# Performance work log

Measured on AMD Instinct MI355X. Metric: run time of the kernel, lower is better.

Reference implementation:

```python
import jax, jax.numpy as jnp
import numpy as np

B, N, IN_DIM = 16, 2048, 64
DIM, HEADS, DEPTH, K, NCLS = 512, 8, 4, 256, 2
DH = DIM // HEADS
EPS = 1e-5


def layernorm(h, s, b):
    mu = jnp.mean(h, axis=-1, keepdims=True)
    var = jnp.mean(jnp.square(h - mu), axis=-1, keepdims=True)
    return (h - mu) * jax.lax.rsqrt(var + EPS) * s + b


def setup_inputs() -> dict:
    key = jax.random.key(0)
    ks = jax.random.split(key, 20)
    w = 0.02
    L = DEPTH
    return {
        "x": jax.random.normal(ks[0], (B, N, IN_DIM), jnp.float32),
        "emb_w": jax.random.normal(ks[1], (IN_DIM, DIM), jnp.float32) * w,
        "emb_b": jnp.zeros((DIM,), jnp.float32),
        "pos": jax.random.normal(ks[2], (1, N, DIM), jnp.float32) * w,
        "ln1_s": jnp.ones((L, DIM), jnp.float32),
        "ln1_b": jnp.zeros((L, DIM), jnp.float32),
        "wq": jax.random.normal(ks[3], (L, DIM, DIM), jnp.float32) * w,
        "wk": jax.random.normal(ks[4], (L, DIM, DIM), jnp.float32) * w,
        "wv": jax.random.normal(ks[5], (L, DIM, DIM), jnp.float32) * w,
        "pk": jax.random.normal(ks[6], (L, N, K), jnp.float32) * (1.0 / np.sqrt(N)),
        "pv": jax.random.normal(ks[7], (L, N, K), jnp.float32) * (1.0 / np.sqrt(N)),
        "wo": jax.random.normal(ks[8], (L, DIM, DIM), jnp.float32) * w,
        "wo_b": jnp.zeros((L, DIM), jnp.float32),
        "ln2_s": jnp.ones((L, DIM), jnp.float32),
        "ln2_b": jnp.zeros((L, DIM), jnp.float32),
        "w1": jax.random.normal(ks[9], (L, DIM, 4 * DIM), jnp.float32) * w,
        "b1": jnp.zeros((L, 4 * DIM), jnp.float32),
        "w2": jax.random.normal(ks[10], (L, 4 * DIM, DIM), jnp.float32) * w,
        "b2": jnp.zeros((L, DIM), jnp.float32),
        "fc_w": jax.random.normal(ks[11], (DIM, NCLS), jnp.float32) * w,
        "fc_b": jnp.zeros((NCLS,), jnp.float32),
    }


def reference(x, emb_w, emb_b, pos, ln1_s, ln1_b, wq, wk, wv, pk, pv, wo, wo_b,
              ln2_s, ln2_b, w1, b1, w2, b2, fc_w, fc_b):
    scale = DH ** -0.5
    h = x @ emb_w + emb_b + pos  # [B,N,DIM]
    for i in range(DEPTH):
        # Linformer self-attention (PreNorm + residual)
        z = layernorm(h, ln1_s[i], ln1_b[i])
        q = (z @ wq[i]).reshape(B, N, HEADS, DH)
        k = z @ wk[i]  # [B,N,DIM]
        v = z @ wv[i]
        # low-rank projection along sequence: [B,N,DIM] x [N,K] -> [B,K,DIM]
        kp = jnp.einsum('bnd,nk->bkd', k, pk[i]).reshape(B, K, HEADS, DH)
        vp = jnp.einsum('bnd,nk->bkd', v, pv[i]).reshape(B, K, HEADS, DH)
        dots = jnp.einsum('bnhd,bkhd->bhnk', q, kp) * scale
        attn = jax.nn.softmax(dots, axis=-1)
        out = jnp.einsum('bhnk,bkhd->bnhd', attn, vp).reshape(B, N, DIM)
        h = h + out @ wo[i] + wo_b[i]
        # FeedForward (PreNorm + residual)
        z = layernorm(h, ln2_s[i], ln2_b[i])
        h = h + jax.nn.gelu(z @ w1[i] + b1[i]) @ w2[i] + b2[i]
    pooled = jnp.mean(h, axis=1)  # [B,DIM]
    return pooled @ fc_w + fc_b  # [B,NCLS]
```

## Files before the change

### kernel.cpp

```cpp
#include <hip/hip_runtime.h>
#include <math.h>

#define B_    16
#define N_    2048
#define INDIM 64
#define DIM_  512
#define HEADS 8
#define DEPTH 4
#define KLIN  256
#define NCLS  2
#define DH    64
#define EPSF  1e-5f

typedef __attribute__((ext_vector_type(8))) short short8v;
typedef __attribute__((ext_vector_type(4))) short short4v;
typedef __attribute__((ext_vector_type(4))) float f32x4;

#define SBAR() __builtin_amdgcn_sched_barrier(0)

__device__ __forceinline__ short f2bf(float f) {
  unsigned u = __float_as_uint(f);
  u += 0x7FFFu + ((u >> 16) & 1u);
  return (short)(u >> 16);
}

__device__ __forceinline__ float wave_sum(float v) {
  #pragma unroll
  for (int o = 32; o > 0; o >>= 1) v += __shfl_xor(v, o);
  return v;
}

__device__ __forceinline__ float gelu_tanh(float x) {
  float u = x * (1.5957691216057308f + 0.07135481627f * x * x);
  return x / (1.f + __expf(-u));
}

__device__ __forceinline__ void gl_lds16(const short* g, short* l) {
  __builtin_amdgcn_global_load_lds(
      (const __attribute__((address_space(1))) unsigned int*)g,
      (__attribute__((address_space(3))) unsigned int*)l, 16, 0, 0);
}

__global__ __launch_bounds__(256) void tconv_k(const float* __restrict__ src,
                                               short* __restrict__ dst, int R,
                                               int C, long long sSrc,
                                               long long sDst) {
  __shared__ float tile[32][33];
  int c0 = blockIdx.x * 32, r0 = blockIdx.y * 32;
  src += (long long)blockIdx.z * sSrc;
  dst += (long long)blockIdx.z * sDst;
  int tx = threadIdx.x & 31, ty = threadIdx.x >> 5;
  #pragma unroll
  for (int rr = 0; rr < 4; ++rr)
    tile[ty + rr * 8][tx] = src[(long long)(r0 + ty + rr * 8) * C + c0 + tx];
  __syncthreads();
  #pragma unroll
  for (int rr = 0; rr < 4; ++rr) {
    int c = ty + rr * 8;
    dst[(long long)(c0 + c) * R + r0 + tx] = f2bf(tile[tx][c]);
  }
}

__global__ __launch_bounds__(256) void cconv_k(const float* __restrict__ src,
                                               short* __restrict__ dst,
                                               int n8) {
  int i = blockIdx.x * 256 + threadIdx.x;
  if (i < n8) {
    const float* s = src + (long long)i * 8;
    float4 a = *(const float4*)s, c = *(const float4*)(s + 4);
    short8v o = {f2bf(a.x), f2bf(a.y), f2bf(a.z), f2bf(a.w),
                 f2bf(c.x), f2bf(c.y), f2bf(c.z), f2bf(c.w)};
    *(short8v*)(dst + (long long)i * 8) = o;
  }
}

__global__ __launch_bounds__(256) void tpose_k(const short* __restrict__ src,
                                               short* __restrict__ dst, int R,
                                               int C, long long sSrc,
                                               long long sDst) {
  __shared__ __align__(16) short tile[64][72];
  int c0 = blockIdx.x * 64, r0 = blockIdx.y * 64;
  src += (long long)blockIdx.z * sSrc;
  dst += (long long)blockIdx.z * sDst;
  int t = threadIdx.x;
  #pragma unroll
  for (int rep = 0; rep < 2; ++rep) {
    int row = rep * 32 + (t >> 3), c8 = (t & 7) * 8;
    *(short8v*)&tile[row][c8] =
        *(const short8v*)(src + (long long)(r0 + row) * C + c0 + c8);
  }
  __syncthreads();
  #pragma unroll
  for (int rep = 0; rep < 2; ++rep) {
    int c = rep * 32 + (t >> 3), r8 = (t & 7) * 8;
    short8v o;
    #pragma unroll
    for (int j = 0; j < 8; ++j) o[j] = tile[r8 + j][c];
    *(short8v*)(dst + (long long)(c0 + c) * R + r0 + r8) = o;
  }
}

__global__ __launch_bounds__(256) void ln_k(const float* __restrict__ h,
                                            const float* __restrict__ s,
                                            const float* __restrict__ b,
                                            short* __restrict__ z) {
  int lane = threadIdx.x & 63;
  long long row = ((long long)blockIdx.x << 2) + (threadIdx.x >> 6);
  const float* hr = h + row * DIM_ + lane * 8;
  float4 a = *(const float4*)hr;
  float4 c = *(const float4*)(hr + 4);
  float sum = a.x + a.y + a.z + a.w + c.x + c.y + c.z + c.w;
  sum = wave_sum(sum);
  float mu = sum * (1.f / DIM_);
  float d[8] = {a.x - mu, a.y - mu, a.z - mu, a.w - mu,
                c.x - mu, c.y - mu, c.z - mu, c.w - mu};
  float vs = 0.f;
  #pragma unroll
  for (int i = 0; i < 8; ++i) vs += d[i] * d[i];
  vs = wave_sum(vs);
  float rstd = rsqrtf(vs * (1.f / DIM_) + EPSF);
  const float* sp = s + lane * 8;
  const float* bp = b + lane * 8;
  float4 s0 = *(const float4*)sp, s1 = *(const float4*)(sp + 4);
  float4 b0 = *(const float4*)bp, b1 = *(const float4*)(bp + 4);
  float o[8];
  o[0] = d[0] * rstd * s0.x + b0.x; o[1] = d[1] * rstd * s0.y + b0.y;
  o[2] = d[2] * rstd * s0.z + b0.z; o[3] = d[3] * rstd * s0.w + b0.w;
  o[4] = d[4] * rstd * s1.x + b1.x; o[5] = d[5] * rstd * s1.y + b1.y;
  o[6] = d[6] * rstd * s1.z + b1.z; o[7] = d[7] * rstd * s1.w + b1.w;
  short8v ov = {f2bf(o[0]), f2bf(o[1]), f2bf(o[2]), f2bf(o[3]),
                f2bf(o[4]), f2bf(o[5]), f2bf(o[6]), f2bf(o[7])};
  *(short8v*)(z + row * DIM_ + lane * 8) = ov;
}

template <int OUTBF, int BM, int BN>
__global__ __launch_bounds__(256) void gemm_bf(
    const short* __restrict__ A, const short* __restrict__ Bsrc,
    const float* __restrict__ bias, const float* __restrict__ resid,
    void* __restrict__ Cv, int M, int N, int K, int lda, int ldb, int ldc,
    long long sAb, long long sBb, long long sCb, int dualThresh,
    long long dualOff, int epi, int resMod) {
  constexpr int MT = BM / 32;
  constexpr int NT = BN / 32;
  constexpr int NLD = BM / 32 + BN / 32;
  int zz = blockIdx.z;
  A += (long long)zz * sAb;
  Bsrc += (long long)zz * sBb;
  int bm = blockIdx.y * BM, bn = blockIdx.x * BN;
  if (dualThresh && bm >= dualThresh) Bsrc += dualOff;
  int t = threadIdx.x;
  __shared__ __align__(16) short Alds[2][BM * 64];
  __shared__ __align__(16) short Blds[2][BN * 64];
  int lane = t & 63, wid = t >> 6;
  int lr = lane & 15, q = lane >> 4;
  int wm = (wid >> 1) * (BM / 2), wn = (wid & 1) * (BN / 2);
  int rl = lane >> 3;
  int cs = (lane & 7) ^ rl;
  f32x4 acc[MT][NT] = {};

  auto stage = [&](int buf, int k0) {
    #pragma unroll
    for (int i = 0; i < BM / 32; ++i) {
      int rb = i * 32 + wid * 8;
      gl_lds16(A + (long long)(bm + rb + rl) * lda + k0 + cs * 8,
               &Alds[buf][rb * 64]);
    }
    #pragma unroll
    for (int i = 0; i < BN / 32; ++i) {
      int rb = i * 32 + wid * 8;
      gl_lds16(Bsrc + (long long)(bn + rb + rl) * ldb + k0 + cs * 8,
               &Blds[buf][rb * 64]);
    }
  };

  stage(0, 0);
  int cur = 0;
  for (int k0 = 0; k0 < K; k0 += 64, cur ^= 1) {
    if (k0 + 64 < K) {
      stage(cur ^ 1, k0 + 64);
      SBAR();
      asm volatile("s_waitcnt vmcnt(%0)" ::"n"(NLD) : "memory");
    } else {
      SBAR();
      asm volatile("s_waitcnt vmcnt(0)" ::: "memory");
    }
    __builtin_amdgcn_s_barrier();
    SBAR();
    #pragma unroll
    for (int kk2 = 0; kk2 < 2; ++kk2) {
      short8v af[MT], bfr[NT];
      #pragma unroll
      for (int mi = 0; mi < MT; ++mi)
        af[mi] = *(const short8v*)&Alds[cur][(wm + mi * 16 + lr) * 64 +
                                             (((kk2 << 2) | q) ^ (lr & 7)) * 8];
      #pragma unroll
      for (int ni = 0; ni < NT; ++ni)
        bfr[ni] = *(const short8v*)&Blds[cur][(wn + ni * 16 + lr) * 64 +
                                              (((kk2 << 2) | q) ^ (lr & 7)) * 8];
      #pragma unroll
      for (int mi = 0; mi < MT; ++mi)
        #pragma unroll
        for (int ni = 0; ni < NT; ++ni)
          acc[mi][ni] = __builtin_amdgcn_mfma_f32_16x16x32_bf16(
              bfr[ni], af[mi], acc[mi][ni], 0, 0, 0);
    }
    SBAR();
    __builtin_amdgcn_s_barrier();
  }

  #pragma unroll
  for (int mi = 0; mi < MT; ++mi) {
    int m = bm + wm + mi * 16 + lr;
    int rm = (epi == 2 && resMod) ? (m % resMod) : m;
    #pragma unroll
    for (int ni = 0; ni < NT; ++ni) {
      int nb = bn + wn + ni * 16 + q * 4;
      f32x4 v = acc[mi][ni];
      if (epi >= 1) {
        float4 bb = *(const float4*)(bias + nb);
        v[0] += bb.x; v[1] += bb.y; v[2] += bb.z; v[3] += bb.w;
      }
      if (epi == 2) {
        float4 rr = *(const float4*)(resid + (long long)rm * ldc + nb);
        v[0] += rr.x; v[1] += rr.y; v[2] += rr.z; v[3] += rr.w;
      } else if (epi == 3) {
        v[0] = gelu_tanh(v[0]); v[1] = gelu_tanh(v[1]);
        v[2] = gelu_tanh(v[2]); v[3] = gelu_tanh(v[3]);
      }
      long long base = (long long)zz * sCb + (long long)m * ldc + nb;
      if (OUTBF) {
        short4v o = {f2bf(v[0]), f2bf(v[1]), f2bf(v[2]), f2bf(v[3])};
        *(short4v*)((short*)Cv + base) = o;
      } else {
        *(float4*)((float*)Cv + base) = make_float4(v[0], v[1], v[2], v[3]);
      }
    }
  }
}

template <int OUTBF, int BN, int EPI>
__global__ __launch_bounds__(512, 2) void gemm8(
    const short* __restrict__ A, const short* __restrict__ Bt,
    const float* __restrict__ bias, const float* __restrict__ resid,
    void* __restrict__ Cv, int M, int N, int K) {
  constexpr int BM = 256;
  constexpr int WCOL = BN / 4;
  constexpr int NT = WCOL / 16;
  constexpr int NTH = NT / 2;
  constexpr int LB = BN / 128;
  __shared__ __align__(16) short Alds[2][BM * 64];
  __shared__ __align__(16) short Blds[2][BN * 64];
  const int tid = threadIdx.x;
  const int lane = tid & 63, wid = tid >> 6;
  const int lr = lane & 15, q = lane >> 4;
  const int wm = (wid >> 2) * 128, wn = (wid & 3) * WCOL;
  const int rl = lane >> 3, cs = (lane & 7) ^ rl;
  const int bm = blockIdx.y * BM, bn = blockIdx.x * BN;
  const short* Ag = A + (long long)bm * K + cs * 8;
  const short* Bg = Bt + (long long)bn * K + cs * 8;
  f32x4 acc[8][NT] = {};

  auto stageA = [&](int slot, int h, int k0) {
    #pragma unroll
    for (int j = 0; j < 2; ++j) {
      int rb = h * 128 + j * 64 + wid * 8;
      gl_lds16(Ag + (long long)(rb + rl) * K + k0, &Alds[slot][rb * 64]);
    }
  };
  auto stageB = [&](int slot, int h, int k0) {
    #pragma unroll
    for (int j = 0; j < LB; ++j) {
      int rb = h * (BN / 2) + j * 64 + wid * 8;
      gl_lds16(Bg + (long long)(rb + rl) * K + k0, &Blds[slot][rb * 64]);
    }
  };
  auto rd = [&](const short* Ls, int row, int kk) -> short8v {
    return *(const short8v*)&Ls[row * 64 + ((((kk << 2) | q) ^ (lr & 7)) << 3)];
  };
  auto mfma4 = [&](short8v (&af)[4][2], short8v (&bf)[NTH][2], int mo, int no) {
    #pragma unroll
    for (int mi = 0; mi < 4; ++mi)
      #pragma unroll
      for (int ni = 0; ni < NTH; ++ni)
        #pragma unroll
        for (int kk = 0; kk < 2; ++kk)
          acc[mo + mi][no + ni] = __builtin_amdgcn_mfma_f32_16x16x32_bf16(
              bf[ni][kk], af[mi][kk], acc[mo + mi][no + ni], 0, 0, 0);
  };

  const int T = K >> 6;
  stageA(0, 0, 0); stageA(0, 1, 0); stageB(0, 0, 0); stageB(0, 1, 0);
  if (T > 1) {
    stageA(1, 0, 64);
    SBAR();
    asm volatile("s_waitcnt vmcnt(2)" ::: "memory");
  } else {
    SBAR();
    asm volatile("s_waitcnt vmcnt(0)" ::: "memory");
  }
  __builtin_amdgcn_s_barrier();

  for (int tt = 0; tt < T; ++tt) {
    const int s = tt & 1, ns = s ^ 1;
    const int kn = (tt + 1) << 6, kn2 = (tt + 2) << 6;
    const short* Als = Alds[s];
    const short* Bls = Blds[s];
    short8v af0[4][2], af1[4][2], bf0[NTH][2], bf1[NTH][2];
    SBAR();
    #pragma unroll
    for (int mi = 0; mi < 4; ++mi)
      #pragma unroll
      for (int kk = 0; kk < 2; ++kk)
        af0[mi][kk] = rd(Als, wm + mi * 16 + lr, kk);
    #pragma unroll
    for (int ni = 0; ni < NTH; ++ni)
      #pragma unroll
      for (int kk = 0; kk < 2; ++kk)
        bf0[ni][kk] = rd(Bls, wn + ni * 16 + lr, kk);
    if (tt + 1 < T) stageA(ns, 1, kn);
    if (BN == 256) asm volatile("s_waitcnt lgkmcnt(8)" ::: "memory");
    SBAR();
    __builtin_amdgcn_s_barrier();
    asm volatile("s_waitcnt lgkmcnt(0)" ::: "memory");
    SBAR();
    __builtin_amdgcn_s_setprio(1);
    mfma4(af0, bf0, 0, 0);
    __builtin_amdgcn_s_setprio(0);
    SBAR();
    __builtin_amdgcn_s_barrier();
    SBAR();
    #pragma unroll
    for (int ni = 0; ni < NTH; ++ni)
      #pragma unroll
      for (int kk = 0; kk < 2; ++kk)
        bf1[ni][kk] = rd(Bls, wn + (NTH + ni) * 16 + lr, kk);
    SBAR();
    __builtin_amdgcn_s_barrier();
    asm volatile("s_waitcnt lgkmcnt(0)" ::: "memory");
    SBAR();
    __builtin_amdgcn_s_setprio(1);
    mfma4(af0, bf1, 0, NTH);
    __builtin_amdgcn_s_setprio(0);
    SBAR();
    __builtin_amdgcn_s_barrier();
    SBAR();
    #pragma unroll
    for (int mi = 0; mi < 4; ++mi)
      #pragma unroll
      for (int kk = 0; kk < 2; ++kk)
        af1[mi][kk] = rd(Als, wm + 64 + mi * 16 + lr, kk);
    if (tt + 1 < T) stageB(ns, 0, kn);
    SBAR();
    __builtin_amdgcn_s_barrier();
    asm volatile("s_waitcnt lgkmcnt(0)" ::: "memory");
    SBAR();
    __builtin_amdgcn_s_setprio(1);
    mfma4(af1, bf0, 4, 0);
    __builtin_amdgcn_s_setprio(0);
    SBAR();
    __builtin_amdgcn_s_barrier();
    SBAR();
    if (tt + 1 < T) stageB(ns, 1, kn);
    if (tt + 2 < T) stageA(s, 0, kn2);
    SBAR();
    __builtin_amdgcn_s_barrier();
    __builtin_amdgcn_s_setprio(1);
    mfma4(af1, bf1, 4, NTH);
    __builtin_amdgcn_s_setprio(0);
    if (tt + 2 < T) {
      SBAR();
      asm volatile("s_waitcnt vmcnt(2)" ::: "memory");
    } else if (tt + 1 < T) {
      SBAR();
      asm volatile("s_waitcnt vmcnt(0)" ::: "memory");
    }
    SBAR();
    __builtin_amdgcn_s_barrier();
  }

  #pragma unroll
  for (int mi = 0; mi < 8; ++mi) {
    int m = bm + wm + mi * 16 + lr;
    #pragma unroll
    for (int nj = 0; nj < NT; ++nj) {
      int nb = bn + wn + nj * 16 + q * 4;
      f32x4 v = acc[mi][nj];
      if (EPI >= 1) {
        float4 bb = *(const float4*)(bias + nb);
        v[0] += bb.x; v[1] += bb.y; v[2] += bb.z; v[3] += bb.w;
      }
      if (EPI == 2) {
        float4 rr = *(const float4*)(resid + (long long)m * N + nb);
        v[0] += rr.x; v[1] += rr.y; v[2] += rr.z; v[3] += rr.w;
      } else if (EPI == 3) {
        v[0] = gelu_tanh(v[0]); v[1] = gelu_tanh(v[1]);
        v[2] = gelu_tanh(v[2]); v[3] = gelu_tanh(v[3]);
      }
      long long base = (long long)m * N + nb;
      if (OUTBF) {
        short4v o = {f2bf(v[0]), f2bf(v[1]), f2bf(v[2]), f2bf(v[3])};
        *(short4v*)((short*)Cv + base) = o;
      } else {
        *(float4*)((float*)Cv + base) = make_float4(v[0], v[1], v[2], v[3]);
      }
    }
  }
}

__global__ __launch_bounds__(256) void attn_k(short* __restrict__ qc,
                                              const short* __restrict__ kvp,
                                              float scale) {
  int n0 = blockIdx.x * 64, hh = blockIdx.y, b = blockIdx.z;
  int t = threadIdx.x;
  int lane = t & 63, w = t >> 6;
  int lr = lane & 15, qd = lane >> 4;

  __shared__ __align__(16) short Qlds[64][72];
  __shared__ __align__(16) short Kbuf[256 * 72];
  __shared__ __align__(16) short Vt[64][264];
  auto Klds = (short(*)[72])Kbuf;
  auto Plds = (short(*)[264])Kbuf;

  short* qptr = qc + (long long)b * N_ * DIM_ + hh * DH;
  const short* kptr = kvp + (long long)b * 2 * KLIN * DIM_ + hh * DH;
  const short* vptr = kptr + (long long)KLIN * DIM_;

  #pragma unroll
  for (int rep = 0; rep < 2; ++rep) {
    int L = rep * 256 + t, row = L >> 3, c8 = (L & 7) << 3;
    *(short8v*)&Qlds[row][c8] =
        *(const short8v*)(qptr + (long long)(n0 + row) * DIM_ + c8);
  }
  #pragma unroll
  for (int rep = 0; rep < 8; ++rep) {
    int L = rep * 256 + t, row = L >> 3, c8 = (L & 7) << 3;
    *(short8v*)&Klds[row][c8] =
        *(const short8v*)(kptr + (long long)row * DIM_ + c8);
  }
  #pragma unroll
  for (int rep = 0; rep < 4; ++rep) {
    int key0 = rep * 64 + (t >> 4) * 4, dh0 = (t & 15) * 4;
    short4v a0 = *(const short4v*)(vptr + (long long)(key0 + 0) * DIM_ + dh0);
    short4v a1 = *(const short4v*)(vptr + (long long)(key0 + 1) * DIM_ + dh0);
    short4v a2 = *(const short4v*)(vptr + (long long)(key0 + 2) * DIM_ + dh0);
    short4v a3 = *(const short4v*)(vptr + (long long)(key0 + 3) * DIM_ + dh0);
    short4v w0 = {a0[0], a1[0], a2[0], a3[0]};
    short4v w1 = {a0[1], a1[1], a2[1], a3[1]};
    short4v w2 = {a0[2], a1[2], a2[2], a3[2]};
    short4v w3 = {a0[3], a1[3], a2[3], a3[3]};
    *(short4v*)&Vt[dh0 + 0][key0] = w0;
    *(short4v*)&Vt[dh0 + 1][key0] = w1;
    *(short4v*)&Vt[dh0 + 2][key0] = w2;
    *(short4v*)&Vt[dh0 + 3][key0] = w3;
  }
  __syncthreads();

  short8v qa0 = *(const short8v*)&Qlds[16 * w + lr][qd * 8];
  short8v qa1 = *(const short8v*)&Qlds[16 * w + lr][32 + qd * 8];
  f32x4 sacc[16];
  #pragma unroll
  for (int nt = 0; nt < 16; ++nt) {
    short8v b0 = *(const short8v*)&Klds[nt * 16 + lr][qd * 8];
    short8v b1 = *(const short8v*)&Klds[nt * 16 + lr][32 + qd * 8];
    f32x4 acc = {};
    acc = __builtin_amdgcn_mfma_f32_16x16x32_bf16(qa0, b0, acc, 0, 0, 0);
    acc = __builtin_amdgcn_mfma_f32_16x16x32_bf16(qa1, b1, acc, 0, 0, 0);
    sacc[nt] = acc;
  }

  #pragma unroll
  for (int r = 0; r < 4; ++r) {
    float m = -1e30f;
    #pragma unroll
    for (int nt = 0; nt < 16; ++nt) {
      sacc[nt][r] *= scale;
      m = fmaxf(m, sacc[nt][r]);
    }
    #pragma unroll
    for (int o = 1; o < 16; o <<= 1) m = fmaxf(m, __shfl_xor(m, o));
    float rs = 0.f;
    #pragma unroll
    for (int nt = 0; nt < 16; ++nt) {
      float e = __expf(sacc[nt][r] - m);
      sacc[nt][r] = e;
      rs += e;
    }
    #pragma unroll
    for (int o = 1; o < 16; o <<= 1) rs += __shfl_xor(rs, o);
    float inv = 1.f / rs;
    #pragma unroll
    for (int nt = 0; nt < 16; ++nt) sacc[nt][r] *= inv;
  }

  __syncthreads();
  #pragma unroll
  for (int nt = 0; nt < 16; ++nt)
    #pragma unroll
    for (int r = 0; r < 4; ++r)
      Plds[16 * w + qd * 4 + r][nt * 16 + lr] = f2bf(sacc[nt][r]);
  __syncthreads();

  f32x4 out[4] = {};
  #pragma unroll
  for (int k0 = 0; k0 < 8; ++k0) {
    short8v ap = *(const short8v*)&Plds[16 * w + lr][k0 * 32 + qd * 8];
    #pragma unroll
    for (int n2 = 0; n2 < 4; ++n2) {
      short8v bv = *(const short8v*)&Vt[n2 * 16 + lr][k0 * 32 + qd * 8];
      out[n2] =
          __builtin_amdgcn_mfma_f32_16x16x32_bf16(bv, ap, out[n2], 0, 0, 0);
    }
  }

  long long rowoff = (long long)(n0 + 16 * w + lr) * DIM_;
  #pragma unroll
  for (int n2 = 0; n2 < 4; ++n2) {
    short4v o = {f2bf(out[n2][0]), f2bf(out[n2][1]), f2bf(out[n2][2]),
                 f2bf(out[n2][3])};
    *(short4v*)(qptr + rowoff + n2 * 16 + qd * 4) = o;
  }
}

__global__ __launch_bounds__(256) void pool1_k(const float* __restrict__ h,
                                               float* __restrict__ partial) {
  int stripe = blockIdx.x, b = blockIdx.y;
  int c4 = (threadIdx.x & 127) * 4, half = threadIdx.x >> 7;
  const float* base =
      h + ((long long)b * N_ + stripe * 128 + half * 64) * DIM_ + c4;
  float4 acc = {0.f, 0.f, 0.f, 0.f};
  for (int r = 0; r < 64; ++r) {
    float4 v = *(const float4*)(base + (long long)r * DIM_);
    acc.x += v.x; acc.y += v.y; acc.z += v.z; acc.w += v.w;
  }
  __shared__ float red[512];
  if (half == 1) *(float4*)&red[c4] = acc;
  __syncthreads();
  if (half == 0) {
    float4 o = *(const float4*)&red[c4];
    o.x += acc.x; o.y += acc.y; o.z += acc.z; o.w += acc.w;
    *(float4*)&partial[((long long)b * 16 + stripe) * DIM_ + c4] = o;
  }
}
__global__ __launch_bounds__(256) void pool2_k(const float* __restrict__ partial,
                                               float* __restrict__ pooled) {
  int b = blockIdx.x;
  for (int c = threadIdx.x; c < DIM_; c += 256) {
    float s = 0.f;
    for (int k = 0; k < 16; ++k) s += partial[((long long)b * 16 + k) * DIM_ + c];
    pooled[b * DIM_ + c] = s * (1.f / N_);
  }
}

__global__ __launch_bounds__(64) void fc_k(const float* __restrict__ pooled,
                                           const float* __restrict__ fc_w,
                                           const float* __restrict__ fc_b,
                                           float* __restrict__ out) {
  int t = threadIdx.x;
  if (t < B_ * NCLS) {
    int b = t >> 1, c = t & 1;
    float s = fc_b[c];
    for (int d = 0; d < DIM_; ++d)
      s += pooled[b * DIM_ + d] * fc_w[d * NCLS + c];
    out[t] = s;
  }
}

extern "C" void kernel_launch(void* const* d_in, const int* in_sizes, int n_in,
                              void* d_out, int out_size, void* d_ws,
                              size_t ws_size, hipStream_t stream) {
  const float* x     = (const float*)d_in[0];
  const float* emb_w = (const float*)d_in[1];
  const float* emb_b = (const float*)d_in[2];
  const float* pos   = (const float*)d_in[3];
  const float* ln1_s = (const float*)d_in[4];
  const float* ln1_b = (const float*)d_in[5];
  const float* wq    = (const float*)d_in[6];
  const float* wk    = (const float*)d_in[7];
  const float* wv    = (const float*)d_in[8];
  const float* pk    = (const float*)d_in[9];
  const float* pv    = (const float*)d_in[10];
  const float* wo    = (const float*)d_in[11];
  const float* wo_b  = (const float*)d_in[12];
  const float* ln2_s = (const float*)d_in[13];
  const float* ln2_b = (const float*)d_in[14];
  const float* w1    = (const float*)d_in[15];
  const float* b1    = (const float*)d_in[16];
  const float* w2    = (const float*)d_in[17];
  const float* b2    = (const float*)d_in[18];
  const float* fc_w  = (const float*)d_in[19];
  const float* fc_b  = (const float*)d_in[20];
  float* out = (float*)d_out;

  const bool big = ws_size >= (size_t)230 * 1024 * 1024;
  const int acb = big ? 16 : 8;
  const long long acrows = (long long)acb * N_;
  const int frows = big ? 16384 : 8192;

  char* P = (char*)d_ws;
  float* h = (float*)P;            P += (long long)B_ * N_ * DIM_ * 4;
  short* zc = (short*)P;           P += acrows * DIM_ * 2;
  short* qc = (short*)P;           P += acrows * DIM_ * 2;
  short* ffnmid = zc;
  short* zcT = (short*)P;          P += acrows * DIM_ * 2;
  short* zln = zcT;
  short* zp = (short*)P;           P += (long long)acb * 2 * KLIN * DIM_ * 2;
  short* kvp = (short*)P;          P += (long long)acb * 2 * KLIN * DIM_ * 2;
  short* wq_t  = (short*)P;  P += (long long)DEPTH * DIM_ * DIM_ * 2;
  short* wkv_t = (short*)P;  P += (long long)DEPTH * 2 * DIM_ * DIM_ * 2;
  short* wo_t  = (short*)P;  P += (long long)DEPTH * DIM_ * DIM_ * 2;
  short* w1_t  = (short*)P;  P += (long long)DEPTH * 4 * DIM_ * DIM_ * 2;
  short* w2_t  = (short*)P;  P += (long long)DEPTH * 4 * DIM_ * DIM_ * 2;
  short* pkv_t = (short*)P;  P += (long long)DEPTH * 2 * KLIN * N_ * 2;
  short* emb_wt = (short*)P; P += (long long)DIM_ * INDIM * 2;
  short* x_bf  = (short*)P;  P += (long long)B_ * N_ * INDIM * 2;
  float* partial = (float*)P; P += (long long)B_ * 16 * DIM_ * 4;
  float* pooled  = (float*)P;

  const float scale = 0.125f;
  const long long WQS = (long long)DIM_ * DIM_;
  const long long KVS = (long long)2 * KLIN * DIM_;

  auto tconv = [&](const float* s, short* d, int R, int C, long long ss,
                   long long sd, int b) {
    hipLaunchKernelGGL(tconv_k, dim3(C / 32, R / 32, b), dim3(256), 0, stream,
                       s, d, R, C, ss, sd);
  };
  tconv(wq, wq_t, DIM_, DIM_, WQS, WQS, DEPTH);
  tconv(wk, wkv_t, DIM_, DIM_, WQS, 2 * WQS, DEPTH);
  tconv(wv, wkv_t + WQS, DIM_, DIM_, WQS, 2 * WQS, DEPTH);
  tconv(wo, wo_t, DIM_, DIM_, WQS, WQS, DEPTH);
  tconv(w1, w1_t, DIM_, 4 * DIM_, 4 * WQS, 4 * WQS, DEPTH);
  tconv(w2, w2_t, 4 * DIM_, DIM_, 4 * WQS, 4 * WQS, DEPTH);
  tconv(pk, pkv_t, N_, KLIN, (long long)N_ * KLIN, (long long)2 * KLIN * N_, DEPTH);
  tconv(pv, pkv_t + (long long)KLIN * N_, N_, KLIN, (long long)N_ * KLIN,
        (long long)2 * KLIN * N_, DEPTH);
  tconv(emb_w, emb_wt, INDIM, DIM_, 0, 0, 1);
  hipLaunchKernelGGL(cconv_k, dim3((B_ * N_ * INDIM / 8 + 255) / 256),
                     dim3(256), 0, stream, x, x_bf, B_ * N_ * INDIM / 8);

  hipLaunchKernelGGL((gemm_bf<0, 128, 128>), dim3(DIM_ / 128, B_ * N_ / 128, 1),
                     dim3(256), 0, stream, x_bf, emb_wt, emb_b, pos, (void*)h,
                     B_ * N_, DIM_, INDIM, INDIM, INDIM, DIM_, 0LL, 0LL, 0LL,
                     0, 0LL, 2, N_);

  for (int i = 0; i < DEPTH; ++i) {
    const short* wq_i  = wq_t + i * WQS;
    const short* wkv_i = wkv_t + i * 2 * WQS;
    const short* wo_i  = wo_t + i * WQS;
    const short* w1_i  = w1_t + (long long)i * 4 * WQS;
    const short* w2_i  = w2_t + (long long)i * 4 * WQS;
    const short* pkv_i = pkv_t + (long long)i * 2 * KLIN * N_;

    for (int c = 0; c < B_ / acb; ++c) {
      float* hc = h + (long long)c * acrows * DIM_;
      hipLaunchKernelGGL(ln_k, dim3(acrows / 4), dim3(256), 0, stream, hc,
                         ln1_s + i * DIM_, ln1_b + i * DIM_, zc);
      hipLaunchKernelGGL(tpose_k, dim3(DIM_ / 64, N_ / 64, acb), dim3(256), 0,
                         stream, zc, zcT, N_, DIM_, (long long)N_ * DIM_,
                         (long long)DIM_ * N_);
      hipLaunchKernelGGL((gemm8<1, 256, 0>),
                         dim3(DIM_ / 256, (int)(acrows / 256), 1), dim3(512), 0,
                         stream, zc, wq_i, nullptr, nullptr, (void*)qc,
                         (int)acrows, DIM_, DIM_);
      hipLaunchKernelGGL((gemm_bf<1, 64, 128>), dim3(DIM_ / 128, 512 / 64, acb),
                         dim3(256), 0, stream, pkv_i, zcT, nullptr, nullptr,
                         (void*)zp, 512, DIM_, N_, N_, N_, DIM_, 0LL,
                         (long long)DIM_ * N_, KVS, 0, 0LL, 0, 0);
      hipLaunchKernelGGL((gemm_bf<1, 64, 128>), dim3(DIM_ / 128, 512 / 64, acb),
                         dim3(256), 0, stream, zp, wkv_i, nullptr, nullptr,
                         (void*)kvp, 512, DIM_, DIM_, DIM_, DIM_, DIM_, KVS,
                         0LL, KVS, KLIN, (long long)WQS, 0, 0);
      hipLaunchKernelGGL(attn_k, dim3(N_ / 64, HEADS, acb), dim3(256), 0,
                         stream, qc, kvp, scale);
      hipLaunchKernelGGL((gemm8<0, 256, 2>),
                         dim3(DIM_ / 256, (int)(acrows / 256), 1), dim3(512), 0,
                         stream, qc, wo_i, wo_b + i * DIM_, hc, (void*)hc,
                         (int)acrows, DIM_, DIM_);
    }

    for (int r0 = 0; r0 < B_ * N_; r0 += frows) {
      float* hr = h + (long long)r0 * DIM_;
      hipLaunchKernelGGL(ln_k, dim3(frows / 4), dim3(256), 0, stream, hr,
                         ln2_s + i * DIM_, ln2_b + i * DIM_, zln);
      hipLaunchKernelGGL((gemm8<1, 256, 3>),
                         dim3(4 * DIM_ / 256, frows / 256, 1), dim3(512), 0,
                         stream, zln, w1_i, b1 + (long long)i * 4 * DIM_,
                         nullptr, (void*)ffnmid, frows, 4 * DIM_, DIM_);
      hipLaunchKernelGGL((gemm8<0, 128, 2>),
                         dim3(DIM_ / 128, frows / 256, 1), dim3(512), 0,
                         stream, ffnmid, w2_i, b2 + (long long)i * DIM_, hr,
                         (void*)hr, frows, DIM_, 4 * DIM_);
    }
  }

  hipLaunchKernelGGL(pool1_k, dim3(16, B_), dim3(256), 0, stream, h, partial);
  hipLaunchKernelGGL(pool2_k, dim3(B_), dim3(256), 0, stream, partial, pooled);
  hipLaunchKernelGGL(fc_k, dim3(1), dim3(64), 0, stream, pooled, fc_w, fc_b,
                     out);
}
```

Measured before the change: 1.988 ms.

## Pre-transpose V for attention, swap MFMA operands, and add XCD block swizzle

Adds a separate transpose kernel that writes V^T into reused zp scratch, so the attention kernel loads V with coalesced 16-byte copies instead of transposing it element-wise in registers. The score MFMA operands are swapped so each lane holds a full query row slice, which cuts softmax reductions to two cross-lane shuffles and allows vectorized short4 stores of P. The gemm8 kernel also remaps block IDs so consecutive tiles are grouped per XCD for better L2 locality. The cost is one extra kernel launch and an extra pass over V per layer chunk.

```diff
diff --git a/kernel.cpp b/kernel.cpp
--- a/kernel.cpp
+++ b/kernel.cpp
@@ -255,7 +255,14 @@
   const int lr = lane & 15, q = lane >> 4;
   const int wm = (wid >> 2) * 128, wn = (wid & 3) * WCOL;
   const int rl = lane >> 3, cs = (lane & 7) ^ rl;
-  const int bm = blockIdx.y * BM, bn = blockIdx.x * BN;
+  const int nwg = gridDim.x * gridDim.y;
+  {
+  }
+  int bid = blockIdx.y * gridDim.x + blockIdx.x;
+  const int nx8 = nwg >> 3, r8 = nwg & 7, xcd = bid & 7, loc = bid >> 3;
+  int swz = (xcd < r8 ? xcd * (nx8 + 1) : r8 * (nx8 + 1) + (xcd - r8) * nx8)
+            + loc;
+  const int bm = (swz / gridDim.x) * BM, bn = (swz % gridDim.x) * BN;
   const short* Ag = A + (long long)bm * K + cs * 8;
   const short* Bg = Bt + (long long)bn * K + cs * 8;
   f32x4 acc[8][NT] = {};
@@ -409,6 +416,7 @@
 
 __global__ __launch_bounds__(256) void attn_k(short* __restrict__ qc,
                                               const short* __restrict__ kvp,
+                                              const short* __restrict__ vt,
                                               float scale) {
   int n0 = blockIdx.x * 64, hh = blockIdx.y, b = blockIdx.z;
   int t = threadIdx.x;
@@ -423,7 +431,7 @@
 
   short* qptr = qc + (long long)b * N_ * DIM_ + hh * DH;
   const short* kptr = kvp + (long long)b * 2 * KLIN * DIM_ + hh * DH;
-  const short* vptr = kptr + (long long)KLIN * DIM_;
+  const short* vtp = vt + (long long)b * DIM_ * KLIN + (long long)hh * DH * KLIN;
 
   #pragma unroll
   for (int rep = 0; rep < 2; ++rep) {
@@ -438,20 +446,10 @@
         *(const short8v*)(kptr + (long long)row * DIM_ + c8);
   }
   #pragma unroll
-  for (int rep = 0; rep < 4; ++rep) {
-    int key0 = rep * 64 + (t >> 4) * 4, dh0 = (t & 15) * 4;
-    short4v a0 = *(const short4v*)(vptr + (long long)(key0 + 0) * DIM_ + dh0);
-    short4v a1 = *(const short4v*)(vptr + (long long)(key0 + 1) * DIM_ + dh0);
-    short4v a2 = *(const short4v*)(vptr + (long long)(key0 + 2) * DIM_ + dh0);
-    short4v a3 = *(const short4v*)(vptr + (long long)(key0 + 3) * DIM_ + dh0);
-    short4v w0 = {a0[0], a1[0], a2[0], a3[0]};
-    short4v w1 = {a0[1], a1[1], a2[1], a3[1]};
-    short4v w2 = {a0[2], a1[2], a2[2], a3[2]};
-    short4v w3 = {a0[3], a1[3], a2[3], a3[3]};
-    *(short4v*)&Vt[dh0 + 0][key0] = w0;
-    *(short4v*)&Vt[dh0 + 1][key0] = w1;
-    *(short4v*)&Vt[dh0 + 2][key0] = w2;
-    *(short4v*)&Vt[dh0 + 3][key0] = w3;
+  for (int rep = 0; rep < 8; ++rep) {
+    int L = rep * 256 + t, row = L >> 5, c8 = (L & 31) << 3;
+    *(short8v*)&Vt[row][c8] =
+        *(const short8v*)(vtp + (long long)row * KLIN + c8);
   }
   __syncthreads();
 
@@ -463,41 +461,38 @@
     short8v b0 = *(const short8v*)&Klds[nt * 16 + lr][qd * 8];
     short8v b1 = *(const short8v*)&Klds[nt * 16 + lr][32 + qd * 8];
     f32x4 acc = {};
-    acc = __builtin_amdgcn_mfma_f32_16x16x32_bf16(qa0, b0, acc, 0, 0, 0);
-    acc = __builtin_amdgcn_mfma_f32_16x16x32_bf16(qa1, b1, acc, 0, 0, 0);
+    acc = __builtin_amdgcn_mfma_f32_16x16x32_bf16(b0, qa0, acc, 0, 0, 0);
+    acc = __builtin_amdgcn_mfma_f32_16x16x32_bf16(b1, qa1, acc, 0, 0, 0);
     sacc[nt] = acc;
   }
 
-  #pragma unroll
-  for (int r = 0; r < 4; ++r) {
-    float m = -1e30f;
-    #pragma unroll
-    for (int nt = 0; nt < 16; ++nt) {
-      sacc[nt][r] *= scale;
-      m = fmaxf(m, sacc[nt][r]);
-    }
-    #pragma unroll
-    for (int o = 1; o < 16; o <<= 1) m = fmaxf(m, __shfl_xor(m, o));
-    float rs = 0.f;
-    #pragma unroll
-    for (int nt = 0; nt < 16; ++nt) {
-      float e = __expf(sacc[nt][r] - m);
+  float mx = -1e30f;
+  #pragma unroll
+  for (int nt = 0; nt < 16; ++nt)
+    #pragma unroll
+    for (int r = 0; r < 4; ++r) mx = fmaxf(mx, sacc[nt][r]);
+  mx = fmaxf(mx, __shfl_xor(mx, 16));
+  mx = fmaxf(mx, __shfl_xor(mx, 32));
+  float rs = 0.f;
+  #pragma unroll
+  for (int nt = 0; nt < 16; ++nt)
+    #pragma unroll
+    for (int r = 0; r < 4; ++r) {
+      float e = __expf((sacc[nt][r] - mx) * scale);
       sacc[nt][r] = e;
       rs += e;
     }
-    #pragma unroll
-    for (int o = 1; o < 16; o <<= 1) rs += __shfl_xor(rs, o);
-    float inv = 1.f / rs;
-    #pragma unroll
-    for (int nt = 0; nt < 16; ++nt) sacc[nt][r] *= inv;
-  }
+  rs += __shfl_xor(rs, 16);
+  rs += __shfl_xor(rs, 32);
+  float inv = 1.f / rs;
 
   __syncthreads();
   #pragma unroll
-  for (int nt = 0; nt < 16; ++nt)
-    #pragma unroll
-    for (int r = 0; r < 4; ++r)
-      Plds[16 * w + qd * 4 + r][nt * 16 + lr] = f2bf(sacc[nt][r]);
+  for (int nt = 0; nt < 16; ++nt) {
+    short4v p = {f2bf(sacc[nt][0] * inv), f2bf(sacc[nt][1] * inv),
+                 f2bf(sacc[nt][2] * inv), f2bf(sacc[nt][3] * inv)};
+    *(short4v*)&Plds[16 * w + lr][nt * 16 + qd * 4] = p;
+  }
   __syncthreads();
 
   f32x4 out[4] = {};
@@ -605,6 +600,7 @@
   short* zln = zcT;
   short* zp = (short*)P;           P += (long long)acb * 2 * KLIN * DIM_ * 2;
   short* kvp = (short*)P;          P += (long long)acb * 2 * KLIN * DIM_ * 2;
+  short* vt = zp;
   short* wq_t  = (short*)P;  P += (long long)DEPTH * DIM_ * DIM_ * 2;
   short* wkv_t = (short*)P;  P += (long long)DEPTH * 2 * DIM_ * DIM_ * 2;
   short* wo_t  = (short*)P;  P += (long long)DEPTH * DIM_ * DIM_ * 2;
@@ -670,8 +666,11 @@
                          dim3(256), 0, stream, zp, wkv_i, nullptr, nullptr,
                          (void*)kvp, 512, DIM_, DIM_, DIM_, DIM_, DIM_, KVS,
                          0LL, KVS, KLIN, (long long)WQS, 0, 0);
+      hipLaunchKernelGGL(tpose_k, dim3(DIM_ / 64, KLIN / 64, acb), dim3(256), 0,
+                         stream, kvp + (long long)KLIN * DIM_, vt, KLIN, DIM_,
+                         KVS, (long long)DIM_ * KLIN);
       hipLaunchKernelGGL(attn_k, dim3(N_ / 64, HEADS, acb), dim3(256), 0,
-                         stream, qc, kvp, scale);
+                         stream, qc, kvp, vt, scale);
       hipLaunchKernelGGL((gemm8<0, 256, 2>),
                          dim3(DIM_ / 256, (int)(acrows / 256), 1), dim3(512), 0,
                          stream, qc, wo_i, wo_b + i * DIM_, hc, (void*)hc,
```

After: 1.896 ms. 4.6% less time.
